# Performance work log

Hardware: AMD Instinct MI355X
Metric: run time of the kernel (lower is better)

## Reference

```python
import jax, jax.numpy as jnp
import numpy as np

INPUT_DIM = 256
OUTPUT_DIM = 256
GRID_SIZE = 32


def setup_inputs() -> dict:
    key = jax.random.key(0)
    k1, k2 = jax.random.split(key)
    x = jax.random.normal(k1, (4096, INPUT_DIM), dtype=jnp.float32)
    # fouriercoeffs: randn(2, out, in, grid) / (sqrt(in) * sqrt(grid))  (smooth_initialization=False)
    scale = np.sqrt(INPUT_DIM) * np.sqrt(GRID_SIZE)
    fouriercoeffs = jax.random.normal(k2, (2, OUTPUT_DIM, INPUT_DIM, GRID_SIZE), dtype=jnp.float32) / scale
    bias = jnp.zeros((1, OUTPUT_DIM), dtype=jnp.float32)
    return {"x": x, "fouriercoeffs": fouriercoeffs, "bias": bias}


def reference(x, fouriercoeffs, bias):
    # x: [N, input_dim]; fouriercoeffs: [2, out, in, grid]; bias: [1, out]
    grid_size = fouriercoeffs.shape[-1]
    k = jnp.arange(1, grid_size + 1, dtype=x.dtype)  # [grid]
    phase = x[:, :, None] * k  # [N, in, grid]
    c = jnp.cos(phase)
    s = jnp.sin(phase)
    # contraction over (in, grid) -> GEMM-like einsum; same math as the
    # original broadcast-multiply-sum but without the [N,out,in,grid] blowup
    y = jnp.einsum("big,jig->bj", c, fouriercoeffs[0])
    y = y + jnp.einsum("big,jig->bj", s, fouriercoeffs[1])
    y = y + bias
    return y
```

## Files before the change

kernel.cpp:

```cpp
#include <hip/hip_runtime.h>
#include <hip/hip_bf16.h>
#include <cstdint>

typedef __attribute__((ext_vector_type(8))) short  short8;
typedef __attribute__((ext_vector_type(4))) float  f32x4;
typedef __attribute__((ext_vector_type(4))) unsigned uint4v;

#define N_ROWS   4096
#define IN_DIM   256
#define OUT_DIM  256
#define K_TOTAL  16384
#define SPLITK   8
#define KCHUNK   2048
#define BM       128
#define BN       128
#define BK       64
#define STEPS    32

#define BMAT_BYTES   (OUT_DIM * K_TOTAL * 2)
#define PART_ELEMS   (N_ROWS * OUT_DIM)
#define WS_NEEDED    (BMAT_BYTES + SPLITK * PART_ELEMS * 4)

__global__ void convert_coeffs(const float* __restrict__ w,
                               __hip_bfloat16* __restrict__ bm) {
    int gid = blockIdx.x * 256 + threadIdx.x;
    int j   = gid >> 11;
    int rem = gid & 2047;
    int i   = rem >> 3;
    int g4  = rem & 7;
    const float* s0 = w + ((size_t)(j * 256 + i)) * 32 + g4 * 4;
    const float* s1 = s0 + (size_t)OUT_DIM * IN_DIM * 32;
    f32x4 c4 = *(const f32x4*)s0;
    f32x4 sn = *(const f32x4*)s1;
    __hip_bfloat16 o[8];
    #pragma unroll
    for (int q = 0; q < 4; ++q) {
        o[2 * q]     = __float2bfloat16(c4[q]);
        o[2 * q + 1] = __float2bfloat16(sn[q]);
    }
    *(short8*)(bm + (size_t)j * K_TOTAL + i * 64 + g4 * 8) = *(short8*)o;
}

__global__ void bias_fill(const float* __restrict__ bias, float* __restrict__ out) {
    int gid = blockIdx.x * 256 + threadIdx.x;
    out[gid] = bias[gid & (OUT_DIM - 1)];
}

__global__ void reduce_out(const float* __restrict__ part,
                           const float* __restrict__ bias,
                           float* __restrict__ out) {
    int gid = blockIdx.x * 256 + threadIdx.x;
    int idx = gid * 4;
    f32x4 a = *(const f32x4*)&bias[idx & (OUT_DIM - 1)];
    #pragma unroll
    for (int ks = 0; ks < SPLITK; ++ks)
        a += *(const f32x4*)&part[(size_t)ks * PART_ELEMS + idx];
    *(f32x4*)&out[idx] = a;
}

__device__ __forceinline__ void gld_lds16(const void* g, void* l) {
    __builtin_amdgcn_global_load_lds(
        (const __attribute__((address_space(1))) void*)(uintptr_t)g,
        (__attribute__((address_space(3))) void*)(uintptr_t)l, 16, 0, 0);
}

__device__ __forceinline__ unsigned packbf(float c, float s) {
    float2 f2; f2.x = c; f2.y = s;
    __hip_bfloat162 pb = __float22bfloat162_rn(f2);
    unsigned u; __builtin_memcpy(&u, &pb, 4);
    return u;
}

template <bool PART>
__global__ __launch_bounds__(256, 2) void fkan_gemm(const float* __restrict__ x,
                                                    const __hip_bfloat16* __restrict__ bm,
                                                    float* __restrict__ dst) {
    __shared__ float  x_lds[STEPS][BM];
    __shared__ short  A_lds[BM * BK];
    __shared__ short  B_lds[2][BN * BK];

    const int tid  = threadIdx.x;
    const int lane = tid & 63;
    const int wid  = tid >> 6;
    const int wm   = wid >> 1;
    const int wn   = wid & 1;

    const int bid = blockIdx.x;
    const int ks  = bid & 7;
    const int tt  = bid >> 3;
    const int mb  = tt >> 1;
    const int nb  = tt & 1;
    const int m0  = mb * BM;
    const int n0  = nb * BN;
    const int i0  = ks * STEPS;
    const int kbase = ks * KCHUNK;

    auto stage_B = [&](int s, int buf) {
        int kg = kbase + s * BK;
        #pragma unroll
        for (int r = 0; r < 4; ++r) {
            int jl = wid * 32 + r * 8 + (lane >> 3);
            int cg = (lane & 7) ^ (jl & 7);
            const __hip_bfloat16* src = bm + (size_t)(n0 + jl) * K_TOTAL + kg + cg * 8;
            gld_lds16(src, &B_lds[buf][(wid * 32 + r * 8) * BK]);
        }
    };

    const int am = tid & 127;
    const int ah = tid >> 7;

    auto gen_A = [&](int s) {
        float xv = x_lds[s][am];
        float t  = xv * 0.15915494309189535f;
        float tb = __builtin_amdgcn_fractf(t);
        float s1 = __builtin_amdgcn_sinf(tb);
        float c1 = __builtin_amdgcn_cosf(tb);
        float tg = (float)(16 * ah + 1) * t;
        float tf = __builtin_amdgcn_fractf(tg);
        float sg = __builtin_amdgcn_sinf(tf);
        float cg = __builtin_amdgcn_cosf(tf);
        unsigned pk[16];
        #pragma unroll
        for (int e = 0; e < 16; ++e) {
            pk[e] = packbf(cg, sg);
            float cn = __builtin_fmaf(cg, c1, -(sg * s1));
            sg       = __builtin_fmaf(sg, c1,  (cg * s1));
            cg = cn;
        }
        int base = am * BK;
        #pragma unroll
        for (int q = 0; q < 4; ++q) {
            uint4v w = {pk[4 * q], pk[4 * q + 1], pk[4 * q + 2], pk[4 * q + 3]};
            *(uint4v*)&A_lds[base + (((4 * ah + q) ^ (am & 7)) << 3)] = w;
        }
    };

    f32x4 acc[4][4];
    #pragma unroll
    for (int a = 0; a < 4; ++a)
        #pragma unroll
        for (int b = 0; b < 4; ++b) acc[a][b] = (f32x4){0.f, 0.f, 0.f, 0.f};

    auto compute = [&](int buf) {
        const int rA = lane & 15;
        const int cA = lane >> 4;
        #pragma unroll
        for (int kf = 0; kf < 2; ++kf) {
            short8 af[4], bf[4];
            #pragma unroll
            for (int mf = 0; mf < 4; ++mf) {
                int row = wm * 64 + mf * 16 + rA;
                int ch  = (kf * 4 + cA) ^ (rA & 7);
                af[mf] = *(const short8*)&A_lds[row * BK + ch * 8];
            }
            #pragma unroll
            for (int nf = 0; nf < 4; ++nf) {
                int row = wn * 64 + nf * 16 + rA;
                int ch  = (kf * 4 + cA) ^ (rA & 7);
                bf[nf] = *(const short8*)&B_lds[buf][row * BK + ch * 8];
            }
            #pragma unroll
            for (int mf = 0; mf < 4; ++mf)
                #pragma unroll
                for (int nf = 0; nf < 4; ++nf)
                    acc[mf][nf] = __builtin_amdgcn_mfma_f32_16x16x32_bf16(
                        af[mf], bf[nf], acc[mf][nf], 0, 0, 0);
        }
    };

    stage_B(0, 0);
    #pragma unroll
    for (int s2 = 0; s2 < 4; ++s2) {
        int slot = tid + s2 * 256;
        int m  = slot >> 3;
        int c4 = slot & 7;
        f32x4 xv = *(const f32x4*)&x[(size_t)(m0 + m) * IN_DIM + i0 + c4 * 4];
        #pragma unroll
        for (int q = 0; q < 4; ++q) x_lds[c4 * 4 + q][m] = xv[q];
    }
    __syncthreads();
    gen_A(0);

    int cur = 0;
    for (int s = 0; s < STEPS; ++s) {
        __syncthreads();
        if (s + 1 < STEPS) stage_B(s + 1, cur ^ 1);
        compute(cur);
        __syncthreads();
        if (s + 1 < STEPS) gen_A(s + 1);
        cur ^= 1;
    }

    const int cl = lane & 15;
    const int rl = (lane >> 4) * 4;
    float* base = PART ? dst + (size_t)ks * PART_ELEMS : dst;
    #pragma unroll
    for (int mf = 0; mf < 4; ++mf) {
        #pragma unroll
        for (int nf = 0; nf < 4; ++nf) {
            int row = m0 + wm * 64 + mf * 16 + rl;
            int col = n0 + wn * 64 + nf * 16 + cl;
            #pragma unroll
            for (int r2 = 0; r2 < 4; ++r2) {
                if (PART)
                    base[(size_t)(row + r2) * OUT_DIM + col] = acc[mf][nf][r2];
                else
                    atomicAdd(&base[(size_t)(row + r2) * OUT_DIM + col], acc[mf][nf][r2]);
            }
        }
    }
}

extern "C" void kernel_launch(void* const* d_in, const int* in_sizes, int n_in,
                              void* d_out, int out_size, void* d_ws, size_t ws_size,
                              hipStream_t stream) {
    const float* x      = (const float*)d_in[0];
    const float* coeffs = (const float*)d_in[1];
    const float* bias   = (const float*)d_in[2];
    float* out = (float*)d_out;
    __hip_bfloat16* bmat = (__hip_bfloat16*)d_ws;
    float* part = (float*)((char*)d_ws + BMAT_BYTES);

    convert_coeffs<<<(OUT_DIM * IN_DIM * 8) / 256, 256, 0, stream>>>(coeffs, bmat);

    const int grid = SPLITK * (N_ROWS / BM) * (OUT_DIM / BN);
    if (ws_size >= (size_t)WS_NEEDED) {
        fkan_gemm<true><<<grid, 256, 0, stream>>>(x, bmat, part);
        reduce_out<<<PART_ELEMS / 4 / 256, 256, 0, stream>>>(part, bias, out);
    } else {
        bias_fill<<<(N_ROWS * OUT_DIM) / 256, 256, 0, stream>>>(bias, out);
        fkan_gemm<false><<<grid, 256, 0, stream>>>(x, bmat, out);
    }
}
```

Before: 118.9 us.

## Generate Fourier A fragments in registers instead of staging through LDS

The shared A tile is removed. Each wave now computes its own cos/sin bf16 MFMA A-fragments directly in registers from x_lds right before the MFMAs. This drops the LDS writes and reads for A and one of the two barriers per K step. In exchange, sin/cos and rotation work is done redundantly by the two waves that share the same rows, and per-lane VALU and transcendental work goes up.

```diff
diff --git a/kernel.cpp b/kernel.cpp
--- a/kernel.cpp
+++ b/kernel.cpp
@@ -76,7 +76,6 @@
                                                     const __hip_bfloat16* __restrict__ bm,
                                                     float* __restrict__ dst) {
     __shared__ float  x_lds[STEPS][BM];
-    __shared__ short  A_lds[BM * BK];
     __shared__ short  B_lds[2][BN * BK];
 
     const int tid  = threadIdx.x;
@@ -106,53 +105,45 @@
         }
     };
 
-    const int am = tid & 127;
-    const int ah = tid >> 7;
-
-    auto gen_A = [&](int s) {
-        float xv = x_lds[s][am];
-        float t  = xv * 0.15915494309189535f;
-        float tb = __builtin_amdgcn_fractf(t);
-        float s1 = __builtin_amdgcn_sinf(tb);
-        float c1 = __builtin_amdgcn_cosf(tb);
-        float tg = (float)(16 * ah + 1) * t;
-        float tf = __builtin_amdgcn_fractf(tg);
-        float sg = __builtin_amdgcn_sinf(tf);
-        float cg = __builtin_amdgcn_cosf(tf);
-        unsigned pk[16];
-        #pragma unroll
-        for (int e = 0; e < 16; ++e) {
-            pk[e] = packbf(cg, sg);
-            float cn = __builtin_fmaf(cg, c1, -(sg * s1));
-            sg       = __builtin_fmaf(sg, c1,  (cg * s1));
-            cg = cn;
-        }
-        int base = am * BK;
-        #pragma unroll
-        for (int q = 0; q < 4; ++q) {
-            uint4v w = {pk[4 * q], pk[4 * q + 1], pk[4 * q + 2], pk[4 * q + 3]};
-            *(uint4v*)&A_lds[base + (((4 * ah + q) ^ (am & 7)) << 3)] = w;
-        }
-    };
-
     f32x4 acc[4][4];
     #pragma unroll
     for (int a = 0; a < 4; ++a)
         #pragma unroll
         for (int b = 0; b < 4; ++b) acc[a][b] = (f32x4){0.f, 0.f, 0.f, 0.f};
 
-    auto compute = [&](int buf) {
-        const int rA = lane & 15;
-        const int cA = lane >> 4;
+    const int rA = lane & 15;
+    const int cA = lane >> 4;
+
+    auto compute = [&](int s, int buf) {
+        short8 af[4][2];
+        #pragma unroll
+        for (int mf = 0; mf < 4; ++mf) {
+            float xv = x_lds[s][wm * 64 + mf * 16 + rA];
+            float t  = xv * 0.15915494309189535f;
+            float tb = __builtin_amdgcn_fractf(t);
+            float s1 = __builtin_amdgcn_sinf(tb);
+            float c1 = __builtin_amdgcn_cosf(tb);
+            #pragma unroll
+            for (int kf = 0; kf < 2; ++kf) {
+                float m1 = (float)(kf * 16 + cA * 4 + 1);
+                float tf = __builtin_amdgcn_fractf(m1 * t);
+                float sg = __builtin_amdgcn_sinf(tf);
+                float cg = __builtin_amdgcn_cosf(tf);
+                unsigned pk[4];
+                #pragma unroll
+                for (int e = 0; e < 4; ++e) {
+                    pk[e] = packbf(cg, sg);
+                    float cn = __builtin_fmaf(cg, c1, -(sg * s1));
+                    sg       = __builtin_fmaf(sg, c1,  (cg * s1));
+                    cg = cn;
+                }
+                uint4v w = {pk[0], pk[1], pk[2], pk[3]};
+                __builtin_memcpy(&af[mf][kf], &w, 16);
+            }
+        }
         #pragma unroll
         for (int kf = 0; kf < 2; ++kf) {
-            short8 af[4], bf[4];
-            #pragma unroll
-            for (int mf = 0; mf < 4; ++mf) {
-                int row = wm * 64 + mf * 16 + rA;
-                int ch  = (kf * 4 + cA) ^ (rA & 7);
-                af[mf] = *(const short8*)&A_lds[row * BK + ch * 8];
-            }
+            short8 bf[4];
             #pragma unroll
             for (int nf = 0; nf < 4; ++nf) {
                 int row = wn * 64 + nf * 16 + rA;
@@ -164,7 +155,7 @@
                 #pragma unroll
                 for (int nf = 0; nf < 4; ++nf)
                     acc[mf][nf] = __builtin_amdgcn_mfma_f32_16x16x32_bf16(
-                        af[mf], bf[nf], acc[mf][nf], 0, 0, 0);
+                        af[mf][kf], bf[nf], acc[mf][nf], 0, 0, 0);
         }
     };
 
@@ -179,15 +170,12 @@
         for (int q = 0; q < 4; ++q) x_lds[c4 * 4 + q][m] = xv[q];
     }
     __syncthreads();
-    gen_A(0);
 
     int cur = 0;
     for (int s = 0; s < STEPS; ++s) {
+        if (s + 1 < STEPS) stage_B(s + 1, cur ^ 1);
+        compute(s, cur);
         __syncthreads();
-        if (s + 1 < STEPS) stage_B(s + 1, cur ^ 1);
-        compute(cur);
-        __syncthreads();
-        if (s + 1 < STEPS) gen_A(s + 1);
         cur ^= 1;
     }
 
```

Result: slower. 131.2 us (+10.4%).

## Load B fragments directly from global into registers, dropping B LDS staging

Applied to the files above, without the earlier changes.

Removes the LDS double buffer for the B operand. Each wave now loads its MFMA B fragments straight from global memory into registers, with a two-way register ping-pong that prefetches the next step while the current one computes. This saves LDS traffic and LDS space, which could allow more occupancy. In exchange, B rows are fetched redundantly by both wm-halves of the block, global loads are less coalesced (16-byte chunks strided across rows), and register pressure rises.

```diff
diff --git a/kernel.cpp b/kernel.cpp
--- a/kernel.cpp
+++ b/kernel.cpp
@@ -58,12 +58,6 @@
     *(f32x4*)&out[idx] = a;
 }
 
-__device__ __forceinline__ void gld_lds16(const void* g, void* l) {
-    __builtin_amdgcn_global_load_lds(
-        (const __attribute__((address_space(1))) void*)(uintptr_t)g,
-        (__attribute__((address_space(3))) void*)(uintptr_t)l, 16, 0, 0);
-}
-
 __device__ __forceinline__ unsigned packbf(float c, float s) {
     float2 f2; f2.x = c; f2.y = s;
     __hip_bfloat162 pb = __float22bfloat162_rn(f2);
@@ -77,7 +71,6 @@
                                                     float* __restrict__ dst) {
     __shared__ float  x_lds[STEPS][BM];
     __shared__ short  A_lds[BM * BK];
-    __shared__ short  B_lds[2][BN * BK];
 
     const int tid  = threadIdx.x;
     const int lane = tid & 63;
@@ -95,15 +88,19 @@
     const int i0  = ks * STEPS;
     const int kbase = ks * KCHUNK;
 
-    auto stage_B = [&](int s, int buf) {
-        int kg = kbase + s * BK;
-        #pragma unroll
-        for (int r = 0; r < 4; ++r) {
-            int jl = wid * 32 + r * 8 + (lane >> 3);
-            int cg = (lane & 7) ^ (jl & 7);
-            const __hip_bfloat16* src = bm + (size_t)(n0 + jl) * K_TOTAL + kg + cg * 8;
-            gld_lds16(src, &B_lds[buf][(wid * 32 + r * 8) * BK]);
-        }
+    const int rA = lane & 15;
+    const int cA = lane >> 4;
+
+    auto loadB = [&](int s, short8* bf) {
+        const size_t kg = (size_t)kbase + s * BK;
+        #pragma unroll
+        for (int kf = 0; kf < 2; ++kf)
+            #pragma unroll
+            for (int nf = 0; nf < 4; ++nf) {
+                int row = n0 + wn * 64 + nf * 16 + rA;
+                bf[kf * 4 + nf] = *(const short8*)
+                    &bm[(size_t)row * K_TOTAL + kg + kf * 32 + cA * 8];
+            }
     };
 
     const int am = tid & 127;
@@ -141,12 +138,10 @@
         #pragma unroll
         for (int b = 0; b < 4; ++b) acc[a][b] = (f32x4){0.f, 0.f, 0.f, 0.f};
 
-    auto compute = [&](int buf) {
-        const int rA = lane & 15;
-        const int cA = lane >> 4;
+    auto compute = [&](const short8* bf) {
         #pragma unroll
         for (int kf = 0; kf < 2; ++kf) {
-            short8 af[4], bf[4];
+            short8 af[4];
             #pragma unroll
             for (int mf = 0; mf < 4; ++mf) {
                 int row = wm * 64 + mf * 16 + rA;
@@ -154,21 +149,14 @@
                 af[mf] = *(const short8*)&A_lds[row * BK + ch * 8];
             }
             #pragma unroll
-            for (int nf = 0; nf < 4; ++nf) {
-                int row = wn * 64 + nf * 16 + rA;
-                int ch  = (kf * 4 + cA) ^ (rA & 7);
-                bf[nf] = *(const short8*)&B_lds[buf][row * BK + ch * 8];
-            }
-            #pragma unroll
             for (int mf = 0; mf < 4; ++mf)
                 #pragma unroll
                 for (int nf = 0; nf < 4; ++nf)
                     acc[mf][nf] = __builtin_amdgcn_mfma_f32_16x16x32_bf16(
-                        af[mf], bf[nf], acc[mf][nf], 0, 0, 0);
+                        af[mf], bf[kf * 4 + nf], acc[mf][nf], 0, 0, 0);
         }
     };
 
-    stage_B(0, 0);
     #pragma unroll
     for (int s2 = 0; s2 < 4; ++s2) {
         int slot = tid + s2 * 256;
@@ -178,17 +166,25 @@
         #pragma unroll
         for (int q = 0; q < 4; ++q) x_lds[c4 * 4 + q][m] = xv[q];
     }
+    short8 bA[8], bB[8];
+    loadB(0, bA);
     __syncthreads();
     gen_A(0);
-
-    int cur = 0;
-    for (int s = 0; s < STEPS; ++s) {
+    __syncthreads();
+
+    for (int s = 0; s < STEPS; s += 2) {
+        loadB(s + 1, bB);
+        compute(bA);
         __syncthreads();
-        if (s + 1 < STEPS) stage_B(s + 1, cur ^ 1);
-        compute(cur);
+        gen_A(s + 1);
         __syncthreads();
-        if (s + 1 < STEPS) gen_A(s + 1);
-        cur ^= 1;
+        if (s + 2 < STEPS) loadB(s + 2, bA);
+        compute(bB);
+        __syncthreads();
+        if (s + 2 < STEPS) {
+            gen_A(s + 2);
+            __syncthreads();
+        }
     }
 
     const int cl = lane & 15;
```

After: 143.2 us. 1.2x slower.

## Widen N tile to full output, double split-K, drop x LDS staging

Applied to the files above, without the earlier changes.

Each block now covers all 256 output columns (BN=256), so the sin/cos A tile is generated once per row block rather than once per N half. Split-K doubles to 16 so the grid keeps the same block count. The x staging through LDS is removed in favour of direct global reads, and the barrier placement in the main loop is restructured. The trade-offs are twice the accumulator registers per thread, a larger B buffer in LDS that may reduce occupancy, and twice the partial-sum traffic through the reduce kernel.

```diff
diff --git a/kernel.cpp b/kernel.cpp
--- a/kernel.cpp
+++ b/kernel.cpp
@@ -10,16 +10,16 @@
 #define IN_DIM   256
 #define OUT_DIM  256
 #define K_TOTAL  16384
-#define SPLITK   8
-#define KCHUNK   2048
+#define SPLITK   16
+#define KCHUNK   1024
 #define BM       128
-#define BN       128
+#define BN       256
 #define BK       64
-#define STEPS    32
+#define STEPS    16
 
 #define BMAT_BYTES   (OUT_DIM * K_TOTAL * 2)
 #define PART_ELEMS   (N_ROWS * OUT_DIM)
-#define WS_NEEDED    (BMAT_BYTES + SPLITK * PART_ELEMS * 4)
+#define WS_NEEDED    (BMAT_BYTES + (size_t)SPLITK * PART_ELEMS * 4)
 
 __global__ void convert_coeffs(const float* __restrict__ w,
                                __hip_bfloat16* __restrict__ bm) {
@@ -75,7 +75,6 @@
 __global__ __launch_bounds__(256, 2) void fkan_gemm(const float* __restrict__ x,
                                                     const __hip_bfloat16* __restrict__ bm,
                                                     float* __restrict__ dst) {
-    __shared__ float  x_lds[STEPS][BM];
     __shared__ short  A_lds[BM * BK];
     __shared__ short  B_lds[2][BN * BK];
 
@@ -86,31 +85,29 @@
     const int wn   = wid & 1;
 
     const int bid = blockIdx.x;
-    const int ks  = bid & 7;
-    const int tt  = bid >> 3;
-    const int mb  = tt >> 1;
-    const int nb  = tt & 1;
+    const int ks  = bid & 15;
+    const int mb  = bid >> 4;
     const int m0  = mb * BM;
-    const int n0  = nb * BN;
     const int i0  = ks * STEPS;
     const int kbase = ks * KCHUNK;
 
     auto stage_B = [&](int s, int buf) {
         int kg = kbase + s * BK;
         #pragma unroll
-        for (int r = 0; r < 4; ++r) {
-            int jl = wid * 32 + r * 8 + (lane >> 3);
+        for (int r = 0; r < 8; ++r) {
+            int jl = wid * 64 + r * 8 + (lane >> 3);
             int cg = (lane & 7) ^ (jl & 7);
-            const __hip_bfloat16* src = bm + (size_t)(n0 + jl) * K_TOTAL + kg + cg * 8;
-            gld_lds16(src, &B_lds[buf][(wid * 32 + r * 8) * BK]);
+            const __hip_bfloat16* src = bm + (size_t)jl * K_TOTAL + kg + cg * 8;
+            gld_lds16(src, &B_lds[buf][(wid * 64 + r * 8) * BK]);
         }
     };
 
     const int am = tid & 127;
     const int ah = tid >> 7;
+    const float* xp = x + (size_t)(m0 + am) * IN_DIM + i0;
 
     auto gen_A = [&](int s) {
-        float xv = x_lds[s][am];
+        float xv = xp[s];
         float t  = xv * 0.15915494309189535f;
         float tb = __builtin_amdgcn_fractf(t);
         float s1 = __builtin_amdgcn_sinf(tb);
@@ -135,59 +132,50 @@
         }
     };
 
-    f32x4 acc[4][4];
+    f32x4 acc[4][8];
     #pragma unroll
     for (int a = 0; a < 4; ++a)
         #pragma unroll
-        for (int b = 0; b < 4; ++b) acc[a][b] = (f32x4){0.f, 0.f, 0.f, 0.f};
+        for (int b = 0; b < 8; ++b) acc[a][b] = (f32x4){0.f, 0.f, 0.f, 0.f};
+
+    const int rA = lane & 15;
+    const int cA = lane >> 4;
 
     auto compute = [&](int buf) {
-        const int rA = lane & 15;
-        const int cA = lane >> 4;
         #pragma unroll
         for (int kf = 0; kf < 2; ++kf) {
-            short8 af[4], bf[4];
+            const int ch = (kf * 4 + cA) ^ (rA & 7);
+            short8 af[4], bf[8];
             #pragma unroll
             for (int mf = 0; mf < 4; ++mf) {
                 int row = wm * 64 + mf * 16 + rA;
-                int ch  = (kf * 4 + cA) ^ (rA & 7);
                 af[mf] = *(const short8*)&A_lds[row * BK + ch * 8];
             }
             #pragma unroll
-            for (int nf = 0; nf < 4; ++nf) {
-                int row = wn * 64 + nf * 16 + rA;
-                int ch  = (kf * 4 + cA) ^ (rA & 7);
+            for (int nf = 0; nf < 8; ++nf) {
+                int row = wn * 128 + nf * 16 + rA;
                 bf[nf] = *(const short8*)&B_lds[buf][row * BK + ch * 8];
             }
             #pragma unroll
             for (int mf = 0; mf < 4; ++mf)
                 #pragma unroll
-                for (int nf = 0; nf < 4; ++nf)
+                for (int nf = 0; nf < 8; ++nf)
                     acc[mf][nf] = __builtin_amdgcn_mfma_f32_16x16x32_bf16(
                         af[mf], bf[nf], acc[mf][nf], 0, 0, 0);
         }
     };
 
     stage_B(0, 0);
-    #pragma unroll
-    for (int s2 = 0; s2 < 4; ++s2) {
-        int slot = tid + s2 * 256;
-        int m  = slot >> 3;
-        int c4 = slot & 7;
-        f32x4 xv = *(const f32x4*)&x[(size_t)(m0 + m) * IN_DIM + i0 + c4 * 4];
-        #pragma unroll
-        for (int q = 0; q < 4; ++q) x_lds[c4 * 4 + q][m] = xv[q];
-    }
+    gen_A(0);
     __syncthreads();
-    gen_A(0);
 
     int cur = 0;
     for (int s = 0; s < STEPS; ++s) {
-        __syncthreads();
         if (s + 1 < STEPS) stage_B(s + 1, cur ^ 1);
         compute(cur);
         __syncthreads();
         if (s + 1 < STEPS) gen_A(s + 1);
+        if (s + 1 < STEPS) __syncthreads();
         cur ^= 1;
     }
 
@@ -197,9 +185,9 @@
     #pragma unroll
     for (int mf = 0; mf < 4; ++mf) {
         #pragma unroll
-        for (int nf = 0; nf < 4; ++nf) {
+        for (int nf = 0; nf < 8; ++nf) {
             int row = m0 + wm * 64 + mf * 16 + rl;
-            int col = n0 + wn * 64 + nf * 16 + cl;
+            int col = wn * 128 + nf * 16 + cl;
             #pragma unroll
             for (int r2 = 0; r2 < 4; ++r2) {
                 if (PART)
@@ -223,8 +211,8 @@
 
     convert_coeffs<<<(OUT_DIM * IN_DIM * 8) / 256, 256, 0, stream>>>(coeffs, bmat);
 
-    const int grid = SPLITK * (N_ROWS / BM) * (OUT_DIM / BN);
-    if (ws_size >= (size_t)WS_NEEDED) {
+    const int grid = SPLITK * (N_ROWS / BM);
+    if (ws_size >= WS_NEEDED) {
         fkan_gemm<true><<<grid, 256, 0, stream>>>(x, bmat, part);
         reduce_out<<<PART_ELEMS / 4 / 256, 256, 0, stream>>>(part, bias, out);
     } else {
```

Result: slower. 123.1 us (+3.5%).
